# Kernel optimization log

Measured on AMD Instinct MI355X. Metric: run time of the kernel, lower is better.

The kernel has to match this reference:

```python
import jax, jax.numpy as jnp
import numpy as np

# DeepSpeed FixedSparsityConfig defaults (attention='unidirectional')
BLOCK = 16
NUM_LOCAL_BLOCKS = 4   # local window = 4 blocks = 64 tokens
D_MODEL = 1024
N_HEADS = 16
HEAD_DIM = D_MODEL // N_HEADS


def _block_layout(seq_len: int) -> np.ndarray:
    """Token-level boolean mask [S,S] from the fixed unidirectional block layout.
    Allowed iff: (same 4-block local window AND block_k <= block_q) OR
                 (block_k % 4 == 3 AND block_k <= block_q)  (causal global column).
    Same layout for every head (different_layout_per_head=False)."""
    nb = seq_len // BLOCK
    r = np.arange(nb)
    causal = r[None, :] <= r[:, None]
    same_win = (r[:, None] // NUM_LOCAL_BLOCKS) == (r[None, :] // NUM_LOCAL_BLOCKS)
    glob = (r[None, :] % NUM_LOCAL_BLOCKS) == (NUM_LOCAL_BLOCKS - 1)
    layout = (same_win & causal) | (glob & causal)
    return np.kron(layout, np.ones((BLOCK, BLOCK), dtype=bool))


def setup_inputs() -> dict:
    key = jax.random.key(0)
    ks = jax.random.split(key, 7)
    B, S = 2, 2048
    init = 1.0 / np.sqrt(D_MODEL)
    x = jax.random.normal(ks[0], (B, S, D_MODEL), jnp.float32)
    key_padding_mask = jnp.zeros((B, S), jnp.float32)  # additive mask ('add' mode)
    Wq = jax.random.normal(ks[1], (D_MODEL, D_MODEL), jnp.float32) * init
    Wk = jax.random.normal(ks[2], (D_MODEL, D_MODEL), jnp.float32) * init
    Wv = jax.random.normal(ks[3], (D_MODEL, D_MODEL), jnp.float32) * init
    bq = jax.random.normal(ks[4], (D_MODEL,), jnp.float32) * 0.01
    bk = jax.random.normal(ks[5], (D_MODEL,), jnp.float32) * 0.01
    bv = jax.random.normal(ks[6], (D_MODEL,), jnp.float32) * 0.01
    return dict(x=x, key_padding_mask=key_padding_mask,
                Wq=Wq, bq=bq, Wk=Wk, bk=bk, Wv=Wv, bv=bv)


def reference(x, key_padding_mask, Wq, bq, Wk, bk, Wv, bv):
    B, S, D = x.shape
    q = (x @ Wq + bq).reshape(B, S, N_HEADS, HEAD_DIM)
    k = (x @ Wk + bk).reshape(B, S, N_HEADS, HEAD_DIM)
    v = (x @ Wv + bv).reshape(B, S, N_HEADS, HEAD_DIM)
    scale = HEAD_DIM ** -0.5  # DeepSpeed scales by head_size**-0.5 inside softmax
    scores = jnp.einsum('bqhd,bkhd->bhqk', q, k) * scale
    scores = scores + key_padding_mask[:, None, None, :]
    mask = jnp.asarray(_block_layout(S))  # [S,S] bool; absent blocks excluded from softmax
    scores = jnp.where(mask[None, None], scores, -jnp.inf)
    attn = jax.nn.softmax(scores, axis=-1)
    out = jnp.einsum('bhqk,bkhd->bqhd', attn, v)
    return out.reshape(B, S, D)
```

## Files before the change

kernel.cpp:

```cpp
#include <hip/hip_runtime.h>
#include <hip/hip_bf16.h>

typedef __bf16 bf16;
typedef __bf16 bf16x4 __attribute__((ext_vector_type(4)));
typedef __bf16 bf16x8 __attribute__((ext_vector_type(8)));
typedef float  f32x4  __attribute__((ext_vector_type(4)));

#define D_MODEL 1024
#define S_LEN   2048
#define BATCH   2
#define NH      16
#define HD      64
#define NX ((size_t)BATCH * S_LEN * D_MODEL)

__device__ inline void gl_lds16(const bf16* g, bf16* l) {
    __builtin_amdgcn_global_load_lds(
        (const __attribute__((address_space(1))) void*)g,
        (__attribute__((address_space(3))) void*)l, 16, 0, 0);
}

__global__ __launch_bounds__(256) void prep(
    const float* __restrict__ x, bf16* __restrict__ xb,
    const float* __restrict__ Wq, const float* __restrict__ Wk,
    const float* __restrict__ Wv, bf16* __restrict__ Wt)
{
    __shared__ bf16 tile[64 * 72];

    if (blockIdx.x < 2048) {
        const size_t base = ((size_t)blockIdx.x * 256 + threadIdx.x) * 8;
        const float4 a = *(const float4*)(x + base);
        const float4 b = *(const float4*)(x + base + 4);
        bf16x8 o;
        o[0] = (bf16)a.x; o[1] = (bf16)a.y; o[2] = (bf16)a.z; o[3] = (bf16)a.w;
        o[4] = (bf16)b.x; o[5] = (bf16)b.y; o[6] = (bf16)b.z; o[7] = (bf16)b.w;
        *(bf16x8*)(xb + base) = o;
        return;
    }

    const int id2 = blockIdx.x - 2048;
    const int z = id2 >> 8;
    const float* W = (z == 0) ? Wq : (z == 1) ? Wk : Wv;
    const int k0 = ((id2 >> 4) & 15) * 64, n0 = (id2 & 15) * 64;

    const int r16 = threadIdx.x >> 4, c4 = (threadIdx.x & 15) << 2;

#pragma unroll
    for (int rr = 0; rr < 4; ++rr) {
        const int row = rr * 16 + r16;
        const float4 v = *(const float4*)(W + (size_t)(k0 + row) * D_MODEL + n0 + c4);
        bf16x4 o; o[0] = (bf16)v.x; o[1] = (bf16)v.y; o[2] = (bf16)v.z; o[3] = (bf16)v.w;
        *(bf16x4*)(tile + row * 72 + c4) = o;
    }
    __syncthreads();
#pragma unroll
    for (int rr = 0; rr < 4; ++rr) {
        const int row = rr * 16 + r16;
        bf16x4 o;
#pragma unroll
        for (int j = 0; j < 4; ++j) o[j] = tile[(c4 + j) * 72 + row];
        *(bf16x4*)(Wt + (size_t)(z * D_MODEL + n0 + row) * D_MODEL + k0 + c4) = o;
    }
}

#define GNT 32

__device__ __forceinline__ void stage_A(
    const bf16* __restrict__ Xb, bf16* __restrict__ sA,
    int m0, int k0, int tid, int wave)
{
    const int ci0 = tid;
    const int r0 = ci0 >> 2, c0 = (ci0 & 3) ^ ((ci0 >> 3) & 3);
    gl_lds16(Xb + (size_t)(m0 + r0) * D_MODEL + k0 + c0 * 8, sA + wave * 512);
    const int ci1 = 512 + tid;
    const int r1 = ci1 >> 2, c1 = (ci1 & 3) ^ ((ci1 >> 3) & 3);
    gl_lds16(Xb + (size_t)(m0 + r1) * D_MODEL + k0 + c1 * 8, sA + 4096 + wave * 512);
}

__device__ __forceinline__ void stage_B(
    const bf16* __restrict__ Wt, bf16* __restrict__ sB,
    int n0, int k0, int tid, int wave, int lane)
{
    const int ci0 = tid;
    const int r0 = ci0 >> 2, c0 = (ci0 & 3) ^ ((ci0 >> 3) & 3);
    gl_lds16(Wt + (size_t)(n0 + r0) * D_MODEL + k0 + c0 * 8, sB + wave * 512);
    const int ci1 = 512 + wave * 32 + lane;
    const int r1 = ci1 >> 2, c1 = (ci1 & 3) ^ ((ci1 >> 3) & 3);
    if (lane < 32)
        gl_lds16(Wt + (size_t)(n0 + r1) * D_MODEL + k0 + c1 * 8, sB + 4096 + wave * 256);
}

template<int VM>
__device__ __forceinline__ void gemm_tile_body(
    const bf16* __restrict__ Xb, const bf16* __restrict__ Wt,
    bf16* __restrict__ As, bf16* __restrict__ Bs,
    int m0, int n0, int t, int tid, int wave, int lane, int wm, int wn,
    int col, int pchunk, f32x4 (&acc)[4][6])
{
    if constexpr (VM == 8)      asm volatile("s_waitcnt vmcnt(8)" ::: "memory");
    else if constexpr (VM == 4) asm volatile("s_waitcnt vmcnt(4)" ::: "memory");
    else                        asm volatile("s_waitcnt vmcnt(0)" ::: "memory");
    asm volatile("s_barrier" ::: "memory");

    const bf16* bufA = As + (t & 3) * 8192;
    const bf16* bufB = Bs + (t & 3) * 6144;
    const bool pf = (t + 3 < GNT);
    const int k3 = (t + 3) * 32;

    if (pf) stage_A(Xb, As + ((t + 3) & 3) * 8192, m0, k3, tid, wave);

    bf16x8 a[4], b[6];
#pragma unroll
    for (int mr = 0; mr < 4; ++mr)
        a[mr] = *(const bf16x8*)(bufA + (wm * 64 + mr * 16 + col) * 32 + pchunk * 8);
#pragma unroll
    for (int nr = 0; nr < 3; ++nr)
        b[nr] = *(const bf16x8*)(bufB + (wn * 96 + nr * 16 + col) * 32 + pchunk * 8);

    __builtin_amdgcn_s_setprio(1);
#pragma unroll
    for (int mr = 0; mr < 4; ++mr)
#pragma unroll
        for (int nr = 0; nr < 3; ++nr)
            acc[mr][nr] = __builtin_amdgcn_mfma_f32_16x16x32_bf16(a[mr], b[nr], acc[mr][nr], 0, 0, 0);
    __builtin_amdgcn_s_setprio(0);

    asm volatile("s_barrier" ::: "memory");
    if (pf) stage_B(Wt, Bs + ((t + 3) & 3) * 6144, n0, k3, tid, wave, lane);
#pragma unroll
    for (int nr = 3; nr < 6; ++nr)
        b[nr] = *(const bf16x8*)(bufB + (wn * 96 + nr * 16 + col) * 32 + pchunk * 8);

    __builtin_amdgcn_s_setprio(1);
#pragma unroll
    for (int mr = 0; mr < 4; ++mr)
#pragma unroll
        for (int nr = 3; nr < 6; ++nr)
            acc[mr][nr] = __builtin_amdgcn_mfma_f32_16x16x32_bf16(a[mr], b[nr], acc[mr][nr], 0, 0, 0);
    __builtin_amdgcn_s_setprio(0);
}

__global__ __launch_bounds__(512, 2) void gemm_qkv_dp(
    const bf16* __restrict__ Xb, const bf16* __restrict__ Wt,
    const float* __restrict__ bq, const float* __restrict__ bk,
    const float* __restrict__ bv, bf16* __restrict__ QKV)
{
    extern __shared__ bf16 smem[];
    bf16* As = smem;
    bf16* Bs = smem + 32768;

    const int bid = blockIdx.x, k = bid & 7, j = bid >> 3;
    const int nx = ((k >> 2) << 3) + (j & 7);
    const int my = ((k & 3) << 2) + (j >> 3);
    const int n0 = nx * 192, m0 = my * 256;

    const int tid = threadIdx.x, wave = tid >> 6, lane = tid & 63;
    const int wm = wave >> 1, wn = wave & 1;
    const int col = lane & 15, quad = lane >> 4;
    const int pchunk = quad ^ ((col >> 1) & 3);

    f32x4 acc[4][6] = {};

    stage_A(Xb, As,         m0,  0, tid, wave);  stage_B(Wt, Bs,         n0,  0, tid, wave, lane);
    stage_A(Xb, As + 8192,  m0, 32, tid, wave);  stage_B(Wt, Bs + 6144,  n0, 32, tid, wave, lane);
    stage_A(Xb, As + 16384, m0, 64, tid, wave);  stage_B(Wt, Bs + 12288, n0, 64, tid, wave, lane);

    for (int t = 0; t < GNT - 2; ++t)
        gemm_tile_body<8>(Xb, Wt, As, Bs, m0, n0, t, tid, wave, lane, wm, wn, col, pchunk, acc);
    gemm_tile_body<4>(Xb, Wt, As, Bs, m0, n0, GNT - 2, tid, wave, lane, wm, wn, col, pchunk, acc);
    gemm_tile_body<0>(Xb, Wt, As, Bs, m0, n0, GNT - 1, tid, wave, lane, wm, wn, col, pchunk, acc);

#pragma unroll
    for (int nr = 0; nr < 6; ++nr) {
        const int cg = n0 + wn * 96 + nr * 16 + col;
        const int z = cg >> 10, c = cg & 1023;
        const float bsv = (z == 0 ? bq : (z == 1 ? bk : bv))[c];
        const float scale = (z == 0) ? 0.125f : 1.0f;
        bf16* C = QKV + (size_t)z * NX;
#pragma unroll
        for (int mr = 0; mr < 4; ++mr)
#pragma unroll
            for (int i = 0; i < 4; ++i) {
                const int rg = m0 + wm * 64 + mr * 16 + quad * 4 + i;
                C[(size_t)rg * D_MODEL + c] = (bf16)((acc[mr][nr][i] + bsv) * scale);
            }
    }
}

__global__ __launch_bounds__(256) void sparse_attn64(
    const bf16* __restrict__ Q, const bf16* __restrict__ Kv,
    const bf16* __restrict__ Vv, const float* __restrict__ kpm,
    float* __restrict__ out)
{
    const int lid = blockIdx.x + 32 * (blockIdx.y + 16 * blockIdx.z);
    const int xk = lid & 7, j = lid >> 3;
    const int pair = xk * 4 + (j & 3);
    const int h = pair & 15, b = pair >> 4;
    const int w = 31 - (j >> 2);

    const int t = threadIdx.x, wavei = t >> 6, lane = t & 63;
    const int col = lane & 15, quad = lane >> 4;
    const int qb = 4 * w + wavei;

    __shared__ bf16 KbS[2][64 * 72];
    __shared__ bf16 VtS[2][64 * 72];
    __shared__ bf16 Ps[4][16 * 72];

    const size_t qrow = ((size_t)(b * S_LEN + qb * 16 + col)) * D_MODEL + h * HD;
    const bf16x8 aq0 = *(const bf16x8*)(Q + qrow + quad * 8);
    const bf16x8 aq1 = *(const bf16x8*)(Q + qrow + 32 + quad * 8);

    f32x4 o[4] = {};
    float lacc[4] = {0.f, 0.f, 0.f, 0.f};

    const int nGlob = (w + 3) >> 2;
    const int niter = nGlob + 1;

    const int srow = t >> 2, sd16 = (t & 3) << 4;
    const int sg = srow >> 4, sr = srow & 15;
    const int p2 = t & 31, dg8 = (t >> 5) << 3;
    const int key0 = 2 * p2, vg = key0 >> 4, vr = key0 & 15;

    auto kb_of = [&](int it, int g) -> int {
        if (it == nGlob) return 4 * w + g;
        const int jj = 4 * it + g;
        return (jj < w) ? (4 * jj + 3) : 3;
    };

    bf16x8 rk0, rk1, rv0, rv1;
    {
        const size_t krow = ((size_t)(b * S_LEN + kb_of(0, sg) * 16 + sr)) * D_MODEL + h * HD + sd16;
        rk0 = *(const bf16x8*)(Kv + krow);
        rk1 = *(const bf16x8*)(Kv + krow + 8);
        const size_t vrow = ((size_t)(b * S_LEN + kb_of(0, vg) * 16 + vr)) * D_MODEL + h * HD + dg8;
        rv0 = *(const bf16x8*)(Vv + vrow);
        rv1 = *(const bf16x8*)(Vv + vrow + D_MODEL);
        *(bf16x8*)(KbS[0] + srow * 72 + sd16)     = rk0;
        *(bf16x8*)(KbS[0] + srow * 72 + sd16 + 8) = rk1;
#pragma unroll
        for (int jj = 0; jj < 8; ++jj) {
            bf16 pr[2] = { rv0[jj], rv1[jj] };
            *(unsigned int*)(VtS[0] + (dg8 + jj) * 72 + key0) = *(unsigned int*)pr;
        }
    }

    for (int it = 0; it < niter; ++it) {
        __syncthreads();
        const int cur = it & 1, nxt = cur ^ 1;
        const bool more = (it + 1 < niter);
        if (more) {
            const size_t krow = ((size_t)(b * S_LEN + kb_of(it + 1, sg) * 16 + sr)) * D_MODEL + h * HD + sd16;
            rk0 = *(const bf16x8*)(Kv + krow);
            rk1 = *(const bf16x8*)(Kv + krow + 8);
            const size_t vrow = ((size_t)(b * S_LEN + kb_of(it + 1, vg) * 16 + vr)) * D_MODEL + h * HD + dg8;
            rv0 = *(const bf16x8*)(Vv + vrow);
            rv1 = *(const bf16x8*)(Vv + vrow + D_MODEL);
        }

        const bf16* Kb = KbS[cur];
        const bf16* Vt = VtS[cur];

        f32x4 s[4];
        float mval[4];
        bool  val[4];
#pragma unroll
        for (int g = 0; g < 4; ++g) {
            int kb;
            if (it == nGlob) { kb = 4 * w + g; val[g] = (g <= wavei); }
            else { const int jj = 4 * it + g; val[g] = (jj < w); kb = val[g] ? (4 * jj + 3) : 3; }
            mval[g] = kpm[b * S_LEN + kb * 16 + col];
            f32x4 z = {};
            const bf16x8 bk0 = *(const bf16x8*)(Kb + (g * 16 + col) * 72 + quad * 8);
            const bf16x8 bk1 = *(const bf16x8*)(Kb + (g * 16 + col) * 72 + 32 + quad * 8);
            __builtin_amdgcn_s_setprio(1);
            z = __builtin_amdgcn_mfma_f32_16x16x32_bf16(aq0, bk0, z, 0, 0, 0);
            s[g] = __builtin_amdgcn_mfma_f32_16x16x32_bf16(aq1, bk1, z, 0, 0, 0);
            __builtin_amdgcn_s_setprio(0);
        }

#pragma unroll
        for (int i = 0; i < 4; ++i) {
#pragma unroll
            for (int g = 0; g < 4; ++g) {
                const float si = val[g] ? (s[g][i] + mval[g]) : -1e30f;
                const float pv = __expf(si);
                lacc[i] += pv;
                Ps[wavei][(quad * 4 + i) * 72 + g * 16 + col] = (bf16)pv;
            }
        }

        const bf16x8 aP0 = *(const bf16x8*)(Ps[wavei] + col * 72 + quad * 8);
        const bf16x8 aP1 = *(const bf16x8*)(Ps[wavei] + col * 72 + 32 + quad * 8);
        __builtin_amdgcn_s_setprio(1);
#pragma unroll
        for (int nt = 0; nt < 4; ++nt) {
            const bf16x8 b0 = *(const bf16x8*)(Vt + (nt * 16 + col) * 72 + quad * 8);
            const bf16x8 b1 = *(const bf16x8*)(Vt + (nt * 16 + col) * 72 + 32 + quad * 8);
            o[nt] = __builtin_amdgcn_mfma_f32_16x16x32_bf16(aP0, b0, o[nt], 0, 0, 0);
            o[nt] = __builtin_amdgcn_mfma_f32_16x16x32_bf16(aP1, b1, o[nt], 0, 0, 0);
        }
        __builtin_amdgcn_s_setprio(0);

        if (more) {
            *(bf16x8*)(KbS[nxt] + srow * 72 + sd16)     = rk0;
            *(bf16x8*)(KbS[nxt] + srow * 72 + sd16 + 8) = rk1;
#pragma unroll
            for (int jj = 0; jj < 8; ++jj) {
                bf16 pr[2] = { rv0[jj], rv1[jj] };
                *(unsigned int*)(VtS[nxt] + (dg8 + jj) * 72 + key0) = *(unsigned int*)pr;
            }
        }
    }

#pragma unroll
    for (int i = 0; i < 4; ++i) {
        float rs = lacc[i];
        rs += __shfl_xor(rs, 1);
        rs += __shfl_xor(rs, 2);
        rs += __shfl_xor(rs, 4);
        rs += __shfl_xor(rs, 8);
        const float inv = 1.0f / rs;
        const int rg = b * S_LEN + qb * 16 + quad * 4 + i;
#pragma unroll
        for (int nt = 0; nt < 4; ++nt)
            out[(size_t)rg * D_MODEL + h * HD + nt * 16 + col] = o[nt][i] * inv;
    }
}

extern "C" void kernel_launch(void* const* d_in, const int* in_sizes, int n_in,
                              void* d_out, int out_size, void* d_ws, size_t ws_size,
                              hipStream_t stream)
{
    const float* x = nullptr; const float* kpm = nullptr;
    const float* Wp[3] = {nullptr, nullptr, nullptr};
    const float* bp[3] = {nullptr, nullptr, nullptr};
    int wn = 0, bn = 0;
    for (int i = 0; i < n_in; ++i) {
        const float* p = (const float*)d_in[i];
        const long s = in_sizes[i];
        if (s == (long)NX)            x = p;
        else if (s == BATCH * S_LEN)  kpm = p;
        else if (s == D_MODEL * D_MODEL && wn < 3) Wp[wn++] = p;
        else if (s == D_MODEL && bn < 3)           bp[bn++] = p;
    }

    bf16* Qb = (bf16*)d_ws;
    bf16* Kb = Qb + NX;
    bf16* Vb = Kb + NX;
    bf16* Xb = (bf16*)d_out;
    bf16* Wt = Xb + NX;
    float* outp = (float*)d_out;

    static bool attr_done = false;
    if (!attr_done) {
        (void)hipFuncSetAttribute(reinterpret_cast<const void*>(gemm_qkv_dp),
                                  hipFuncAttributeMaxDynamicSharedMemorySize, 114688);
        attr_done = true;
    }

    prep<<<2816, 256, 0, stream>>>(x, Xb, Wp[0], Wp[1], Wp[2], Wt);

    gemm_qkv_dp<<<dim3(256), 512, 114688, stream>>>(
        Xb, Wt, bp[0], bp[1], bp[2], Qb);

    sparse_attn64<<<dim3(S_LEN / 64, NH, BATCH), 256, 0, stream>>>(
        Qb, Kb, Vb, kpm, outp);
}
```

Baseline: 140.0 us.

## Load K fragments directly into registers and drop the shared K buffer

The attention kernel no longer stages K through double-buffered shared memory. Each wave now loads its MFMA K fragments straight from global memory into registers, one iteration ahead, and prefetches the key-padding mask values along with them. Launch bounds now request 4 blocks per SM. This removes the LDS writes and reads for K and cuts shared memory use, which could allow more occupancy. The cost is that every wave loads the same K rows redundantly (four times the global and L2 traffic for K) and register pressure goes up.

After: 150.5 us. 1.07x slower.

```diff
diff --git a/kernel.cpp b/kernel.cpp
--- a/kernel.cpp
+++ b/kernel.cpp
@@ -186,7 +186,7 @@
     }
 }
 
-__global__ __launch_bounds__(256) void sparse_attn64(
+__global__ __launch_bounds__(256, 4) void sparse_attn64(
     const bf16* __restrict__ Q, const bf16* __restrict__ Kv,
     const bf16* __restrict__ Vv, const float* __restrict__ kpm,
     float* __restrict__ out)
@@ -201,7 +201,6 @@
     const int col = lane & 15, quad = lane >> 4;
     const int qb = 4 * w + wavei;
 
-    __shared__ bf16 KbS[2][64 * 72];
     __shared__ bf16 VtS[2][64 * 72];
     __shared__ bf16 Ps[4][16 * 72];
 
@@ -215,27 +214,30 @@
     const int nGlob = (w + 3) >> 2;
     const int niter = nGlob + 1;
 
-    const int srow = t >> 2, sd16 = (t & 3) << 4;
-    const int sg = srow >> 4, sr = srow & 15;
     const int p2 = t & 31, dg8 = (t >> 5) << 3;
     const int key0 = 2 * p2, vg = key0 >> 4, vr = key0 & 15;
 
     auto kb_of = [&](int it, int g) -> int {
-        if (it == nGlob) return 4 * w + g;
+        if (it >= nGlob) return 4 * w + g;
         const int jj = 4 * it + g;
         return (jj < w) ? (4 * jj + 3) : 3;
     };
 
-    bf16x8 rk0, rk1, rv0, rv1;
+    bf16x8 kf0[4], kf1[4], rv0, rv1;
+    float mnext[4], mval[4];
+
     {
-        const size_t krow = ((size_t)(b * S_LEN + kb_of(0, sg) * 16 + sr)) * D_MODEL + h * HD + sd16;
-        rk0 = *(const bf16x8*)(Kv + krow);
-        rk1 = *(const bf16x8*)(Kv + krow + 8);
         const size_t vrow = ((size_t)(b * S_LEN + kb_of(0, vg) * 16 + vr)) * D_MODEL + h * HD + dg8;
         rv0 = *(const bf16x8*)(Vv + vrow);
         rv1 = *(const bf16x8*)(Vv + vrow + D_MODEL);
-        *(bf16x8*)(KbS[0] + srow * 72 + sd16)     = rk0;
-        *(bf16x8*)(KbS[0] + srow * 72 + sd16 + 8) = rk1;
+#pragma unroll
+        for (int g = 0; g < 4; ++g) {
+            const int kb = kb_of(0, g);
+            const size_t kr = ((size_t)(b * S_LEN + kb * 16 + col)) * D_MODEL + h * HD + quad * 8;
+            kf0[g] = *(const bf16x8*)(Kv + kr);
+            kf1[g] = *(const bf16x8*)(Kv + kr + 32);
+            mnext[g] = kpm[b * S_LEN + kb * 16 + col];
+        }
 #pragma unroll
         for (int jj = 0; jj < 8; ++jj) {
             bf16 pr[2] = { rv0[jj], rv1[jj] };
@@ -247,34 +249,35 @@
         __syncthreads();
         const int cur = it & 1, nxt = cur ^ 1;
         const bool more = (it + 1 < niter);
+
+#pragma unroll
+        for (int g = 0; g < 4; ++g) mval[g] = mnext[g];
+
+        f32x4 s[4];
+        bool  val[4];
+#pragma unroll
+        for (int g = 0; g < 4; ++g) {
+            if (it == nGlob) val[g] = (g <= wavei);
+            else             val[g] = (4 * it + g < w);
+            f32x4 z = {};
+            __builtin_amdgcn_s_setprio(1);
+            z = __builtin_amdgcn_mfma_f32_16x16x32_bf16(aq0, kf0[g], z, 0, 0, 0);
+            s[g] = __builtin_amdgcn_mfma_f32_16x16x32_bf16(aq1, kf1[g], z, 0, 0, 0);
+            __builtin_amdgcn_s_setprio(0);
+        }
+
         if (more) {
-            const size_t krow = ((size_t)(b * S_LEN + kb_of(it + 1, sg) * 16 + sr)) * D_MODEL + h * HD + sd16;
-            rk0 = *(const bf16x8*)(Kv + krow);
-            rk1 = *(const bf16x8*)(Kv + krow + 8);
             const size_t vrow = ((size_t)(b * S_LEN + kb_of(it + 1, vg) * 16 + vr)) * D_MODEL + h * HD + dg8;
             rv0 = *(const bf16x8*)(Vv + vrow);
             rv1 = *(const bf16x8*)(Vv + vrow + D_MODEL);
-        }
-
-        const bf16* Kb = KbS[cur];
-        const bf16* Vt = VtS[cur];
-
-        f32x4 s[4];
-        float mval[4];
-        bool  val[4];
-#pragma unroll
-        for (int g = 0; g < 4; ++g) {
-            int kb;
-            if (it == nGlob) { kb = 4 * w + g; val[g] = (g <= wavei); }
-            else { const int jj = 4 * it + g; val[g] = (jj < w); kb = val[g] ? (4 * jj + 3) : 3; }
-            mval[g] = kpm[b * S_LEN + kb * 16 + col];
-            f32x4 z = {};
-            const bf16x8 bk0 = *(const bf16x8*)(Kb + (g * 16 + col) * 72 + quad * 8);
-            const bf16x8 bk1 = *(const bf16x8*)(Kb + (g * 16 + col) * 72 + 32 + quad * 8);
-            __builtin_amdgcn_s_setprio(1);
-            z = __builtin_amdgcn_mfma_f32_16x16x32_bf16(aq0, bk0, z, 0, 0, 0);
-            s[g] = __builtin_amdgcn_mfma_f32_16x16x32_bf16(aq1, bk1, z, 0, 0, 0);
-            __builtin_amdgcn_s_setprio(0);
+#pragma unroll
+            for (int g = 0; g < 4; ++g) {
+                const int kb = kb_of(it + 1, g);
+                const size_t kr = ((size_t)(b * S_LEN + kb * 16 + col)) * D_MODEL + h * HD + quad * 8;
+                kf0[g] = *(const bf16x8*)(Kv + kr);
+                kf1[g] = *(const bf16x8*)(Kv + kr + 32);
+                mnext[g] = kpm[b * S_LEN + kb * 16 + col];
+            }
         }
 
 #pragma unroll
@@ -288,6 +291,7 @@
             }
         }
 
+        const bf16* Vt = VtS[cur];
         const bf16x8 aP0 = *(const bf16x8*)(Ps[wavei] + col * 72 + quad * 8);
         const bf16x8 aP1 = *(const bf16x8*)(Ps[wavei] + col * 72 + 32 + quad * 8);
         __builtin_amdgcn_s_setprio(1);
@@ -301,8 +305,6 @@
         __builtin_amdgcn_s_setprio(0);
 
         if (more) {
-            *(bf16x8*)(KbS[nxt] + srow * 72 + sd16)     = rk0;
-            *(bf16x8*)(KbS[nxt] + srow * 72 + sd16 + 8) = rk1;
 #pragma unroll
             for (int jj = 0; jj < 8; ++jj) {
                 bf16 pr[2] = { rv0[jj], rv1[jj] };
```

## Single-buffer K tile, skip masked score blocks, and set occupancy launch bound

Applied to the files above, without the earlier changes.

Drops the double buffer for the K tile. The next K tile is now written into the single buffer after an extra barrier placed mid-iteration, once all waves have read scores. This frees LDS, and a launch bound of 4 blocks per CU is added to favour occupancy. The score MFMAs and exponentials are also skipped for invalid key blocks, writing zeros to P instead. The extra barrier per iteration adds synchronisation cost, and the per-block branches may cause divergence overhead.

New measurement: 135.5 us. 3.2% less time.

```diff
diff --git a/kernel.cpp b/kernel.cpp
--- a/kernel.cpp
+++ b/kernel.cpp
@@ -186,7 +186,7 @@
     }
 }
 
-__global__ __launch_bounds__(256) void sparse_attn64(
+__global__ __launch_bounds__(256, 4) void sparse_attn64(
     const bf16* __restrict__ Q, const bf16* __restrict__ Kv,
     const bf16* __restrict__ Vv, const float* __restrict__ kpm,
     float* __restrict__ out)
@@ -201,7 +201,7 @@
     const int col = lane & 15, quad = lane >> 4;
     const int qb = 4 * w + wavei;
 
-    __shared__ bf16 KbS[2][64 * 72];
+    __shared__ bf16 KbS[64 * 72];
     __shared__ bf16 VtS[2][64 * 72];
     __shared__ bf16 Ps[4][16 * 72];
 
@@ -221,7 +221,7 @@
     const int key0 = 2 * p2, vg = key0 >> 4, vr = key0 & 15;
 
     auto kb_of = [&](int it, int g) -> int {
-        if (it == nGlob) return 4 * w + g;
+        if (it >= nGlob) return 4 * w + g;
         const int jj = 4 * it + g;
         return (jj < w) ? (4 * jj + 3) : 3;
     };
@@ -234,8 +234,8 @@
         const size_t vrow = ((size_t)(b * S_LEN + kb_of(0, vg) * 16 + vr)) * D_MODEL + h * HD + dg8;
         rv0 = *(const bf16x8*)(Vv + vrow);
         rv1 = *(const bf16x8*)(Vv + vrow + D_MODEL);
-        *(bf16x8*)(KbS[0] + srow * 72 + sd16)     = rk0;
-        *(bf16x8*)(KbS[0] + srow * 72 + sd16 + 8) = rk1;
+        *(bf16x8*)(KbS + srow * 72 + sd16)     = rk0;
+        *(bf16x8*)(KbS + srow * 72 + sd16 + 8) = rk1;
 #pragma unroll
         for (int jj = 0; jj < 8; ++jj) {
             bf16 pr[2] = { rv0[jj], rv1[jj] };
@@ -256,38 +256,48 @@
             rv1 = *(const bf16x8*)(Vv + vrow + D_MODEL);
         }
 
-        const bf16* Kb = KbS[cur];
-        const bf16* Vt = VtS[cur];
-
         f32x4 s[4];
         float mval[4];
         bool  val[4];
 #pragma unroll
         for (int g = 0; g < 4; ++g) {
-            int kb;
-            if (it == nGlob) { kb = 4 * w + g; val[g] = (g <= wavei); }
-            else { const int jj = 4 * it + g; val[g] = (jj < w); kb = val[g] ? (4 * jj + 3) : 3; }
-            mval[g] = kpm[b * S_LEN + kb * 16 + col];
-            f32x4 z = {};
-            const bf16x8 bk0 = *(const bf16x8*)(Kb + (g * 16 + col) * 72 + quad * 8);
-            const bf16x8 bk1 = *(const bf16x8*)(Kb + (g * 16 + col) * 72 + 32 + quad * 8);
-            __builtin_amdgcn_s_setprio(1);
-            z = __builtin_amdgcn_mfma_f32_16x16x32_bf16(aq0, bk0, z, 0, 0, 0);
-            s[g] = __builtin_amdgcn_mfma_f32_16x16x32_bf16(aq1, bk1, z, 0, 0, 0);
-            __builtin_amdgcn_s_setprio(0);
-        }
-
-#pragma unroll
-        for (int i = 0; i < 4; ++i) {
-#pragma unroll
-            for (int g = 0; g < 4; ++g) {
-                const float si = val[g] ? (s[g][i] + mval[g]) : -1e30f;
-                const float pv = __expf(si);
-                lacc[i] += pv;
-                Ps[wavei][(quad * 4 + i) * 72 + g * 16 + col] = (bf16)pv;
+            val[g] = (it == nGlob) ? (g <= wavei) : (4 * it + g < w);
+            if (val[g]) {
+                const int kb = kb_of(it, g);
+                mval[g] = kpm[b * S_LEN + kb * 16 + col];
+                f32x4 z = {};
+                const bf16x8 bk0 = *(const bf16x8*)(KbS + (g * 16 + col) * 72 + quad * 8);
+                const bf16x8 bk1 = *(const bf16x8*)(KbS + (g * 16 + col) * 72 + 32 + quad * 8);
+                __builtin_amdgcn_s_setprio(1);
+                z = __builtin_amdgcn_mfma_f32_16x16x32_bf16(aq0, bk0, z, 0, 0, 0);
+                s[g] = __builtin_amdgcn_mfma_f32_16x16x32_bf16(aq1, bk1, z, 0, 0, 0);
+                __builtin_amdgcn_s_setprio(0);
             }
         }
 
+        __syncthreads();
+        if (more) {
+            *(bf16x8*)(KbS + srow * 72 + sd16)     = rk0;
+            *(bf16x8*)(KbS + srow * 72 + sd16 + 8) = rk1;
+        }
+
+#pragma unroll
+        for (int g = 0; g < 4; ++g) {
+            if (val[g]) {
+#pragma unroll
+                for (int i = 0; i < 4; ++i) {
+                    const float pv = __expf(s[g][i] + mval[g]);
+                    lacc[i] += pv;
+                    Ps[wavei][(quad * 4 + i) * 72 + g * 16 + col] = (bf16)pv;
+                }
+            } else {
+#pragma unroll
+                for (int i = 0; i < 4; ++i)
+                    Ps[wavei][(quad * 4 + i) * 72 + g * 16 + col] = (bf16)0.0f;
+            }
+        }
+
+        const bf16* Vt = VtS[cur];
         const bf16x8 aP0 = *(const bf16x8*)(Ps[wavei] + col * 72 + quad * 8);
         const bf16x8 aP1 = *(const bf16x8*)(Ps[wavei] + col * 72 + 32 + quad * 8);
         __builtin_amdgcn_s_setprio(1);
@@ -301,8 +311,6 @@
         __builtin_amdgcn_s_setprio(0);
 
         if (more) {
-            *(bf16x8*)(KbS[nxt] + srow * 72 + sd16)     = rk0;
-            *(bf16x8*)(KbS[nxt] + srow * 72 + sd16 + 8) = rk1;
 #pragma unroll
             for (int jj = 0; jj < 8; ++jj) {
                 bf16 pr[2] = { rv0[jj], rv1[jj] };
```
